# Performance work log

Hardware: AMD Instinct MI355X
Metric: run time of the kernel (lower is better)

## Reference

```python
import jax, jax.numpy as jnp
import numpy as np
from jax.scipy.linalg import expm

N_WIRES = 9
N_LAYERS = 4
EMBED = 512
BATCH = 64
D = 2 ** N_WIRES
P = N_WIRES * N_LAYERS * 2  # gate angles per sample


def _apply_gate(st, g, w):
    # st: (D, 2,...,2) complex64; apply 2x2 gate g on wire w
    st = jnp.moveaxis(st, 1 + w, -1)
    st = st @ g.T  # new[a] = sum_b g[a,b] old[b]
    return jnp.moveaxis(st, -1, 1 + w)


def _apply_cnot(st, c, t):
    st = jnp.moveaxis(st, (1 + c, 1 + t), (-2, -1))
    st = jnp.concatenate([st[..., 0:1, :], st[..., 1:2, ::-1]], axis=-2)
    return jnp.moveaxis(st, (-2, -1), (1 + c, 1 + t))


def _build_unitary(params):
    # simulate circuit on all D basis states at once (identity input)
    st = jnp.eye(D, dtype=jnp.complex64).reshape((D,) + (2,) * N_WIRES)
    idx = 0
    for _ in range(N_LAYERS):
        for w in range(N_WIRES):
            thy = params[idx]
            thz = params[idx + 1]
            idx += 2
            c = jnp.cos(thy * 0.5).astype(jnp.complex64)
            s = jnp.sin(thy * 0.5).astype(jnp.complex64)
            ry = jnp.stack([jnp.stack([c, -s]), jnp.stack([s, c])])
            ep = jnp.exp(0.5j * thz.astype(jnp.complex64))  # exp(i*thz/2)
            zero = jnp.zeros((), jnp.complex64)
            rz = jnp.stack([jnp.stack([jnp.conj(ep), zero]), jnp.stack([zero, ep])])
            st = _apply_gate(st, rz @ ry, w)  # Ry then Rz, fused
        for w in range(N_WIRES - 1):
            st = _apply_cnot(st, w, w + 1)
        st = _apply_cnot(st, N_WIRES - 1, 0)  # ring entangler (n_wires>1)
    # row index = input basis state i -> column i of U; take real part
    return jnp.real(st.reshape(D, D)).T


def _forward(t, w1, b1, w2, b2):
    h = jax.nn.silu(t[:, None] @ w1 + b1)          # (B, EMBED)
    params = h @ w2 + b2                            # (B, P)
    p_sg = jax.lax.stop_gradient(params)            # torch uses .detach() for the circuit
    U_stack = jax.vmap(_build_unitary)(p_sg)        # (B, D, D)
    B = t.shape[0]
    A = jnp.zeros((B, D * D), params.dtype).at[:, :P].set(params).reshape(B, D, D)
    A_skew = (A - jnp.swapaxes(A, -1, -2)) * 0.01
    U_diff = jax.vmap(expm)(A_skew)                 # (B, D, D)
    return jnp.einsum('bij,bjk->bik', U_stack, U_diff)


def setup_inputs() -> dict:
    key = jax.random.key(0)
    k_t, k1, kb1, k2, kb2 = jax.random.split(key, 5)
    t = jax.random.normal(k_t, (BATCH,), jnp.float32)
    w1 = jax.random.normal(k1, (1, EMBED), jnp.float32)
    b1 = jax.random.normal(kb1, (EMBED,), jnp.float32) * 0.1
    w2 = jax.random.normal(k2, (EMBED, P), jnp.float32) / np.sqrt(EMBED)
    b2 = jax.random.normal(kb2, (P,), jnp.float32) * 0.1
    return {"t": t, "w1": w1, "b1": b1, "w2": w2, "b2": b2}


def reference(t, w1, b1, w2, b2):
    return _forward(t, w1, b1, w2, b2)
```

## Files before the change

### kernel.cpp

```cpp
#include <hip/hip_runtime.h>
#include <math.h>


#define PSTRIDE 2560
#define GD_OFF  0
#define SC_OFF  144
#define L_OFF(l) (160 + (l)*256)
#define V_OFF   1184
#define W_OFF   1280
#define C0_OFF  1792

__device__ __forceinline__ float2 cmul(float2 a, float2 b){
  return make_float2(fmaf(a.x, b.x, -a.y*b.y), fmaf(a.x, b.y, a.y*b.x));
}

__device__ __forceinline__ float2 pk_fma_s_lo(float2 s2, float2 b, float2 c){
  float2 d;
  asm("v_pk_fma_f32 %0, %1, %2, %3 op_sel:[0,0,0] op_sel_hi:[0,1,1]"
      : "=v"(d) : "s"(s2), "v"(b), "v"(c));
  return d;
}
__device__ __forceinline__ float2 pk_mul_s_hi(float2 s2, float2 b){
  float2 d;
  asm("v_pk_mul_f32 %0, %1, %2 op_sel:[1,0] op_sel_hi:[1,1]"
      : "=v"(d) : "s"(s2), "v"(b));
  return d;
}
__device__ __forceinline__ float2 pk_mul_s_lo(float2 s2, float2 b){
  float2 d;
  asm("v_pk_mul_f32 %0, %1, %2 op_sel:[0,0] op_sel_hi:[0,1]"
      : "=v"(d) : "s"(s2), "v"(b));
  return d;
}
__device__ __forceinline__ float2 pk_fma_vs_lo(float2 a, float2 b, float2 c){
  float2 d;
  asm("v_pk_fma_f32 %0, %1, %2, %3 op_sel:[0,0,0] op_sel_hi:[0,1,1]"
      : "=v"(d) : "v"(a), "s"(b), "v"(c));
  return d;
}
__device__ __forceinline__ float2 pk_mul_vs_hi(float2 a, float2 b){
  float2 d;
  asm("v_pk_mul_f32 %0, %1, %2 op_sel:[1,0] op_sel_hi:[1,1]"
      : "=v"(d) : "v"(a), "s"(b));
  return d;
}
__device__ __forceinline__ float2 pk_fma_vv_lo(float2 a, float2 b, float2 c){
  float2 d;
  asm("v_pk_fma_f32 %0, %1, %2, %3 op_sel:[0,0,0] op_sel_hi:[0,1,1]"
      : "=v"(d) : "v"(a), "v"(b), "v"(c));
  return d;
}
__device__ __forceinline__ float2 pk_mul_vv_hi(float2 a, float2 b){
  float2 d;
  asm("v_pk_mul_f32 %0, %1, %2 op_sel:[1,0] op_sel_hi:[1,1]"
      : "=v"(d) : "v"(a), "v"(b));
  return d;
}
__device__ __forceinline__ float2 pk_swapneg(float2 c, float2 n){
  float2 d;
  asm("v_pk_mul_f32 %0, %1, %2 op_sel:[1,0] op_sel_hi:[0,1]"
      : "=v"(d) : "v"(c), "v"(n));
  return d;
}

template<int OFS>
__device__ __forceinline__ float2 swz2(float2 v){
  const int x = __builtin_amdgcn_ds_swizzle(__float_as_int(v.x), OFS);
  const int y = __builtin_amdgcn_ds_swizzle(__float_as_int(v.y), OFS);
  return make_float2(__int_as_float(x), __int_as_float(y));
}
template<int CTRL>
__device__ __forceinline__ float2 dpp2(float2 v){
  const int x = __builtin_amdgcn_mov_dpp(__float_as_int(v.x), CTRL, 0xF, 0xF, true);
  const int y = __builtin_amdgcn_mov_dpp(__float_as_int(v.y), CTRL, 0xF, 0xF, true);
  return make_float2(__int_as_float(x), __int_as_float(y));
}

__device__ __forceinline__ int Fperm(int x){
  int S = x ^ (x >> 1); S ^= S >> 2; S ^= S >> 4; S ^= S >> 8;
  return (S & 0xFF) | ((((x >> 8) ^ S) & 1) << 8);
}
__device__ __forceinline__ int physmap(int x){ return x ^ ((x >> 4) & 15); }

template<int STRIDE, bool UNIF>
__device__ __forceinline__ void apply_rot(float2 amp[8], const float* rp){
  const float2 R0 = ((const float2*)rp)[0];
  const float2 R1 = ((const float2*)rp)[1];
  #pragma unroll
  for (int b = 0; b < 8; ++b){
    if (b & STRIDE) continue;
    const float2 u = amp[b], v = amp[b + STRIDE];
    if constexpr (UNIF){
      amp[b]          = pk_fma_s_lo(R0, u, pk_mul_s_hi(R0, v));
      amp[b + STRIDE] = pk_fma_s_lo(R1, u, pk_mul_s_hi(R1, v));
    } else {
      amp[b]          = pk_fma_vv_lo(R0, u, pk_mul_vv_hi(R0, v));
      amp[b + STRIDE] = pk_fma_vv_lo(R1, u, pk_mul_vv_hi(R1, v));
    }
  }
}

__device__ __forceinline__ void run_layer2(float2* __restrict__ S,
    const float* __restrict__ lb, const int lane,
    const int base1, const int base2, const int base3, const int baseF,
    const float2 NEG1P1){
  float2 amp[8];
  #pragma unroll
  for (int j = 0; j < 8; ++j) amp[j] = S[base1 ^ j];
  apply_rot<4,false>(amp, lb + 6*4);
  apply_rot<2,false>(amp, lb + 7*4);
  apply_rot<1,false>(amp, lb + 8*4);
  #pragma unroll
  for (int j = 0; j < 8; ++j) S[base1 ^ j] = amp[j];
  #pragma unroll
  for (int j = 0; j < 8; ++j) amp[j] = S[base2 ^ ((j << 3) ^ (j >> 1))];
  apply_rot<4,false>(amp, lb + 3*4);
  apply_rot<2,false>(amp, lb + 4*4);
  apply_rot<1,false>(amp, lb + 5*4);
  #pragma unroll
  for (int j = 0; j < 8; ++j) S[base2 ^ ((j << 3) ^ (j >> 1))] = amp[j];
  #pragma unroll
  for (int j = 0; j < 8; ++j) amp[j] = S[base3 ^ ((j << 6) ^ ((4*j) & 15))];
  apply_rot<4,false>(amp, lb + 0*4);
  apply_rot<2,false>(amp, lb + 1*4);
  apply_rot<1,false>(amp, lb + 2*4);
  {
    const float2 A  = *(const float2*)(lb + 128 + lane*2);
    const float2 A2 = pk_swapneg(A, NEG1P1);
    #pragma unroll
    for (int j = 0; j < 8; ++j)
      amp[j] = pk_fma_vv_lo(amp[j], A, pk_mul_vv_hi(amp[j], A2));
    #pragma unroll
    for (int j = 0; j < 8; ++j){
      const float2 P = *(const float2*)(lb + 64 + j*4);
      const float2 Q = *(const float2*)(lb + 64 + j*4 + 2);
      amp[j] = pk_fma_vv_lo(amp[j], P, pk_mul_vv_hi(amp[j], Q));
    }
  }
  #pragma unroll
  for (int j = 0; j < 8; ++j) S[baseF ^ physmap(Fperm(j << 6))] = amp[j];
}

#define XROT(GET, RP, BIT) {                                        \
    const float2 R0 = ((const float2*)(RP))[0];    \
    const float2 R1 = ((const float2*)(RP))[1];    \
    const float  Bs = (BIT) ? R1.x : R0.y;                          \
    const float2 Bv = make_float2(Bs, Bs);                          \
    _Pragma("unroll")                                               \
    for (int j = 0; j < 8; ++j){                                    \
      const float2 p = GET(amp[j]);                                 \
      amp[j] = pk_fma_vv_lo(Bv, p, pk_mul_s_lo(R0, amp[j]));        \
    }                                                               \
  }

__device__ __forceinline__ void run_layer_h(float2* __restrict__ S,
    const float* __restrict__ lb, const int lane,
    const int base1, const int base3, const int baseF,
    const float2 NEG1P1){
  float2 amp[8];
  #pragma unroll
  for (int j = 0; j < 8; ++j) amp[j] = S[base1 ^ j];
  apply_rot<4,true>(amp, lb + 6*4);
  apply_rot<2,true>(amp, lb + 7*4);
  apply_rot<1,true>(amp, lb + 8*4);
  XROT(swz2<0x101F>, lb + 3*4, (lane >> 2) & 1);
  XROT(dpp2<0x4E>,   lb + 4*4, (lane >> 1) & 1);
  XROT(dpp2<0xB1>,   lb + 5*4, lane & 1);
  #pragma unroll
  for (int j = 0; j < 8; ++j) S[base1 ^ j] = amp[j];
  #pragma unroll
  for (int j = 0; j < 8; ++j) amp[j] = S[base3 ^ ((j << 6) ^ ((4*j) & 15))];
  apply_rot<4,true>(amp, lb + 0*4);
  apply_rot<2,true>(amp, lb + 1*4);
  apply_rot<1,true>(amp, lb + 2*4);
  {
    const float2 A  = *(const float2*)(lb + 128 + lane*2);
    const float2 A2 = pk_swapneg(A, NEG1P1);
    #pragma unroll
    for (int j = 0; j < 8; ++j)
      amp[j] = pk_fma_vv_lo(amp[j], A, pk_mul_vv_hi(amp[j], A2));
    #pragma unroll
    for (int j = 0; j < 8; ++j){
      const float2 P = *(const float2*)(lb + 64 + j*4);
      const float2 Q = *(const float2*)(lb + 64 + j*4 + 2);
      amp[j] = pk_fma_vs_lo(amp[j], P, pk_mul_vs_hi(amp[j], Q));
    }
  }
  #pragma unroll
  for (int j = 0; j < 8; ++j) S[baseF ^ physmap(Fperm(j << 6))] = amp[j];
}

__global__ __launch_bounds__(576)
void prep_kernel(const float* __restrict__ t,  const float* __restrict__ w1,
                 const float* __restrict__ b1, const float* __restrict__ w2,
                 const float* __restrict__ b2, float* __restrict__ prep){
  __shared__ float sh[512];
  __shared__ float part[8][72];
  __shared__ float spar[72];
  __shared__ float tl[4][256];
  __shared__ float ssc[3];
  __shared__ __align__(16) float2 vst[2][512];
  const int s = blockIdx.x;
  const float ts = t[s];
  for (int k = threadIdx.x; k < 512; k += 576){
    const float z = fmaf(ts, w1[k], b1[k]);
    sh[k] = z / (1.f + expf(-z));
  }
  __syncthreads();
  {
    const int p = threadIdx.x % 72, c = threadIdx.x / 72;
    float acc = 0.f;
    const int k0 = c*64;
    for (int k = k0; k < k0 + 64; ++k) acc = fmaf(sh[k], w2[k*72 + p], acc);
    part[c][p] = acc;
  }
  __syncthreads();
  if (threadIdx.x < 72){
    const int p = threadIdx.x;
    float acc = b2[p];
    #pragma unroll
    for (int c = 0; c < 8; ++c) acc += part[c][p];
    spar[p] = acc;
  }
  __syncthreads();
  float* pb = prep + (size_t)s*PSTRIDE;
  const int tid = threadIdx.x;
  if (tid < 256){
    const int l = tid >> 6, m = tid & 63;
    float2 acc = make_float2(1.f, 0.f);
    #pragma unroll
    for (int w = 3; w < 9; ++w){
      const float thz = spar[2*(9*l + w) + 1];
      float zi, zr; sincosf(0.5f*thz, &zi, &zr);
      const int bit = (m >> (8 - w)) & 1;
      acc = cmul(acc, make_float2(zr, bit ? zi : -zi));
    }
    pb[L_OFF(l) + 128 + 2*m]     = acc.x;
    pb[L_OFF(l) + 128 + 2*m + 1] = acc.y;
    tl[l][128 + 2*m]     = acc.x;
    tl[l][128 + 2*m + 1] = acc.y;
  } else if (tid < 288){
    const int q = tid - 256, l = q >> 3, j = q & 7;
    float2 acc = make_float2(1.f, 0.f);
    #pragma unroll
    for (int w = 0; w < 3; ++w){
      const float thz = spar[2*(9*l + w) + 1];
      float zi, zr; sincosf(0.5f*thz, &zi, &zr);
      const int bit = (j >> (2 - w)) & 1;
      acc = cmul(acc, make_float2(zr, bit ? zi : -zi));
    }
    float* o = pb + L_OFF(l) + 64 + j*4;
    o[0] = acc.x; o[1] = acc.y; o[2] = -acc.y; o[3] = acc.x;
    float* o2 = &tl[l][64 + j*4];
    o2[0] = acc.x; o2[1] = acc.y; o2[2] = -acc.y; o2[3] = acc.x;
  } else if (tid < 324){
    const int q = tid - 288, l = q / 9, w = q - l*9;
    const float thy = spar[2*(9*l + w)];
    float sy, cy; sincosf(0.5f*thy, &sy, &cy);
    float* o = pb + L_OFF(l) + w*4;
    o[0] = cy; o[1] = -sy; o[2] = sy; o[3] = cy;
    float* o2 = &tl[l][w*4];
    o2[0] = cy; o2[1] = -sy; o2[2] = sy; o2[3] = cy;
  } else if (tid < 333){
    const int w = tid - 324;
    const float thy = spar[2*w], thz = spar[2*w + 1];
    float sy, cy, zi, zr;
    sincosf(0.5f*thy, &sy, &cy);
    sincosf(0.5f*thz, &zi, &zr);
    const float gr[4] = { zr*cy, -zr*sy, zr*sy, zr*cy };
    const float gi[4] = { -zi*cy, zi*sy, zi*sy, zi*cy };
    float* o = pb + GD_OFF + w*16;
    #pragma unroll
    for (int e = 0; e < 4; ++e){
      o[e*4+0] = gr[e]; o[e*4+1] = gi[e]; o[e*4+2] = -gi[e]; o[e*4+3] = gr[e];
    }
  } else if (tid < 405){
    const int j = tid - 333;
    pb[V_OFF + j] = (j == 0) ? 0.f : 0.01f*spar[j];
  } else if (tid == 405){
    float th2 = 0.f;
    for (int j = 1; j < 72; ++j){ const float v = 0.01f*spar[j]; th2 = fmaf(v, v, th2); }
    const float th = sqrtf(th2);
    float alpha, beta;
    if (th > 1e-6f){
      alpha = sinf(th)/th;
      const float s2 = sinf(0.5f*th);
      beta = 2.f*s2*s2/th2;
    } else { alpha = 1.f - th2/6.f; beta = 0.5f; }
    pb[SC_OFF+0] = cosf(th);
    pb[SC_OFF+1] = alpha;
    pb[SC_OFF+2] = beta;
    ssc[0] = cosf(th); ssc[1] = alpha; ssc[2] = beta;
  }
  __syncthreads();
  if (tid < 128){
    const int wv = tid >> 6, lane = tid & 63;
    float2* const S = vst[wv];
    const float2 NEG1P1 = make_float2(-1.f, 1.f);
    const int base1 = (lane << 3) ^ ((lane >> 1) & 15);
    const int hq = lane >> 3, lq = lane & 7;
    const int base2 = (hq << 6) ^ ((hq << 2) & 15) ^ lq;
    const int base3 = lane ^ (lane >> 4);
    const int baseF = physmap(Fperm(lane));
    #pragma unroll
    for (int j = 0; j < 8; ++j){
      const int x = (lane << 3) + j;
      float re;
      if (wv == 0) re = (x == 0) ? 1.f : 0.f;
      else         re = (x >= 1 && x < 72) ? 0.01f*spar[x] : 0.f;
      S[base1 ^ j] = make_float2(re, 0.f);
    }
    #pragma unroll
    for (int L = 0; L < 4; ++L)
      run_layer2(S, &tl[L][0], lane, base1, base2, base3, baseF, NEG1P1);
  }
  __syncthreads();
  if (tid < 512){
    const int a  = tid;
    const int pa = a ^ ((a >> 4) & 15);
    const float u0 = vst[0][pa].x;
    const float uv = vst[1][pa].x;
    pb[W_OFF  + a] = fmaf(ssc[1], u0, -ssc[2]*uv);
    pb[C0_OFF + a] = fmaf(ssc[0], u0, -ssc[1]*uv);
  }
}

__global__ __launch_bounds__(512, 6)
void sim_kernel(const float* __restrict__ prep, float* __restrict__ out){
  __shared__ __align__(16) float2 st[8][512];
  const int s    = blockIdx.x & 63;
  const int cb   = blockIdx.x >> 6;
  const int wid  = threadIdx.x >> 6;
  const int lane = threadIdx.x & 63;
  const int col  = cb*8 + wid;
  const float* gp = prep + (size_t)s*PSTRIDE;
  float2* const S = st[wid];
  const float2 NEG1P1 = make_float2(-1.f, 1.f);

  float2 amp[8];
  {
    float2 base = make_float2(1.f, 0.f);
    #pragma unroll
    for (int w = 0; w < 6; ++w){
      const int xb = (lane >> (5 - w)) & 1;
      const int ib = (col  >> (8 - w)) & 1;
      const float4 gd = *(const float4*)(gp + GD_OFF + w*16 + (xb*2 + ib)*4);
      const float2 d1 = make_float2(gd.x, gd.y);
      const float2 d2 = make_float2(gd.z, gd.w);
      base = pk_fma_vv_lo(base, d1, pk_mul_vv_hi(base, d2));
    }
    const int i6 = (col >> 2) & 1, i7 = (col >> 1) & 1, i8 = col & 1;
    float2 g6[2]; float4 g7d[2], g8d[2];
    #pragma unroll
    for (int r = 0; r < 2; ++r){
      g6[r]  = *(const float2*)(gp + GD_OFF + 6*16 + (r*2 + i6)*4);
      g7d[r] = *(const float4*)(gp + GD_OFF + 7*16 + (r*2 + i7)*4);
      g8d[r] = *(const float4*)(gp + GD_OFF + 8*16 + (r*2 + i8)*4);
    }
    float2 g67[4];
    #pragma unroll
    for (int a = 0; a < 2; ++a){
      #pragma unroll
      for (int b = 0; b < 2; ++b){
        const float2 d1 = make_float2(g7d[b].x, g7d[b].y);
        const float2 d2 = make_float2(g7d[b].z, g7d[b].w);
        g67[a*2+b] = pk_fma_vv_lo(g6[a], d1, pk_mul_vv_hi(g6[a], d2));
      }
    }
    const float2 bd2 = pk_swapneg(base, NEG1P1);
    #pragma unroll
    for (int j = 0; j < 8; ++j){
      const float4 g8 = g8d[j & 1];
      const float2 e1 = make_float2(g8.x, g8.y);
      const float2 e2 = make_float2(g8.z, g8.w);
      const float2 T  = pk_fma_vv_lo(g67[j >> 1], e1, pk_mul_vv_hi(g67[j >> 1], e2));
      amp[j] = pk_fma_vv_lo(T, base, pk_mul_vv_hi(T, bd2));
    }
    const int bFI = physmap(Fperm(lane << 3));
    #pragma unroll
    for (int j = 0; j < 8; ++j) S[bFI ^ physmap(Fperm(j))] = amp[j];
  }

  const int base1 = (lane << 3) ^ ((lane >> 1) & 15);
  const int base3 = lane ^ (lane >> 4);
  const int baseF = physmap(Fperm(lane));

  run_layer_h(S, gp + L_OFF(1), lane, base1, base3, baseF, NEG1P1);
  run_layer_h(S, gp + L_OFF(2), lane, base1, base3, baseF, NEG1P1);
  run_layer_h(S, gp + L_OFF(3), lane, base1, base3, baseF, NEG1P1);

  __syncthreads();
  const float* wt  = gp + W_OFF;
  const float* c0t = gp + C0_OFF;
  const float* vt  = gp + V_OFF;
  #pragma unroll
  for (int rep = 0; rep < 2; ++rep){
    const int a  = (threadIdx.x >> 1) + rep*256;
    const int q  = threadIdx.x & 1;
    const int pa = a ^ ((a >> 4) & 15);
    float4 vv;
    vv.x = st[q*4 + 0][pa].x;
    vv.y = st[q*4 + 1][pa].x;
    vv.z = st[q*4 + 2][pa].x;
    vv.w = st[q*4 + 3][pa].x;
    if (cb < 9){
      const float  wa = wt[a];
      const float4 vj = *(const float4*)(vt + cb*8 + q*4);
      vv.x = fmaf(wa, vj.x, vv.x);
      vv.y = fmaf(wa, vj.y, vv.y);
      vv.z = fmaf(wa, vj.z, vv.z);
      vv.w = fmaf(wa, vj.w, vv.w);
      if ((cb | q) == 0) vv.x = c0t[a];
    }
    *(float4*)&out[(size_t)s*262144 + (size_t)a*512 + cb*8 + q*4] = vv;
  }
}

extern "C" void kernel_launch(void* const* d_in, const int* in_sizes, int n_in,
                              void* d_out, int out_size, void* d_ws, size_t ws_size,
                              hipStream_t stream){
  const float* t  = (const float*)d_in[0];
  const float* w1 = (const float*)d_in[1];
  const float* b1 = (const float*)d_in[2];
  const float* w2 = (const float*)d_in[3];
  const float* b2 = (const float*)d_in[4];
  float* out  = (float*)d_out;
  float* prep = (float*)d_ws;
  prep_kernel<<<64,   576, 0, stream>>>(t, w1, b1, w2, b2, prep);
  sim_kernel <<<4096, 512, 0, stream>>>(prep, out);
}
```

Baseline: 143.2 us.

## Replace mid-layer LDS transpose with cross-lane rotations for high wires

New measurement: 146.9 us. 2.6% more time.

```diff
diff --git a/kernel.cpp b/kernel.cpp
--- a/kernel.cpp
+++ b/kernel.cpp
@@ -73,6 +73,11 @@
 __device__ __forceinline__ float2 dpp2(float2 v){
   const int x = __builtin_amdgcn_mov_dpp(__float_as_int(v.x), CTRL, 0xF, 0xF, true);
   const int y = __builtin_amdgcn_mov_dpp(__float_as_int(v.y), CTRL, 0xF, 0xF, true);
+  return make_float2(__int_as_float(x), __int_as_float(y));
+}
+__device__ __forceinline__ float2 bperm2(int addr, float2 v){
+  const int x = __builtin_amdgcn_ds_bpermute(addr, __float_as_int(v.x));
+  const int y = __builtin_amdgcn_ds_bpermute(addr, __float_as_int(v.y));
   return make_float2(__int_as_float(x), __int_as_float(y));
 }
 
@@ -141,21 +146,21 @@
   for (int j = 0; j < 8; ++j) S[baseF ^ physmap(Fperm(j << 6))] = amp[j];
 }
 
-#define XROT(GET, RP, BIT) {                                        \
+#define XROT(GETEXPR, RP, BIT) {                                    \
     const float2 R0 = ((const float2*)(RP))[0];    \
     const float2 R1 = ((const float2*)(RP))[1];    \
     const float  Bs = (BIT) ? R1.x : R0.y;                          \
     const float2 Bv = make_float2(Bs, Bs);                          \
     _Pragma("unroll")                                               \
     for (int j = 0; j < 8; ++j){                                    \
-      const float2 p = GET(amp[j]);                                 \
+      const float2 p = GETEXPR;                                     \
       amp[j] = pk_fma_vv_lo(Bv, p, pk_mul_s_lo(R0, amp[j]));        \
     }                                                               \
   }
 
-__device__ __forceinline__ void run_layer_h(float2* __restrict__ S,
+__device__ __forceinline__ void run_layer_r(float2* __restrict__ S,
     const float* __restrict__ lb, const int lane,
-    const int base1, const int base3, const int baseF,
+    const int base1, const int bFI, const int bpaddr,
     const float2 NEG1P1){
   float2 amp[8];
   #pragma unroll
@@ -163,16 +168,12 @@
   apply_rot<4,true>(amp, lb + 6*4);
   apply_rot<2,true>(amp, lb + 7*4);
   apply_rot<1,true>(amp, lb + 8*4);
-  XROT(swz2<0x101F>, lb + 3*4, (lane >> 2) & 1);
-  XROT(dpp2<0x4E>,   lb + 4*4, (lane >> 1) & 1);
-  XROT(dpp2<0xB1>,   lb + 5*4, lane & 1);
-  #pragma unroll
-  for (int j = 0; j < 8; ++j) S[base1 ^ j] = amp[j];
-  #pragma unroll
-  for (int j = 0; j < 8; ++j) amp[j] = S[base3 ^ ((j << 6) ^ ((4*j) & 15))];
-  apply_rot<4,true>(amp, lb + 0*4);
-  apply_rot<2,true>(amp, lb + 1*4);
-  apply_rot<1,true>(amp, lb + 2*4);
+  XROT(swz2<0x101F>(amp[j]), lb + 3*4, (lane >> 2) & 1);
+  XROT(dpp2<0x4E>(amp[j]),   lb + 4*4, (lane >> 1) & 1);
+  XROT(dpp2<0xB1>(amp[j]),   lb + 5*4, lane & 1);
+  XROT(bperm2(bpaddr, amp[j]), lb + 0*4, (lane >> 5) & 1);
+  XROT(swz2<0x401F>(amp[j]),   lb + 1*4, (lane >> 4) & 1);
+  XROT(swz2<0x201F>(amp[j]),   lb + 2*4, (lane >> 3) & 1);
   {
     const float2 A  = *(const float2*)(lb + 128 + lane*2);
     const float2 A2 = pk_swapneg(A, NEG1P1);
@@ -187,7 +188,7 @@
     }
   }
   #pragma unroll
-  for (int j = 0; j < 8; ++j) S[baseF ^ physmap(Fperm(j << 6))] = amp[j];
+  for (int j = 0; j < 8; ++j) S[bFI ^ physmap(Fperm(j))] = amp[j];
 }
 
 __global__ __launch_bounds__(576)
@@ -235,10 +236,18 @@
       const int bit = (m >> (8 - w)) & 1;
       acc = cmul(acc, make_float2(zr, bit ? zi : -zi));
     }
-    pb[L_OFF(l) + 128 + 2*m]     = acc.x;
-    pb[L_OFF(l) + 128 + 2*m + 1] = acc.y;
     tl[l][128 + 2*m]     = acc.x;
     tl[l][128 + 2*m + 1] = acc.y;
+    float2 dl = make_float2(1.f, 0.f);
+    #pragma unroll
+    for (int w = 0; w < 6; ++w){
+      const float thz = spar[2*(9*l + w) + 1];
+      float zi, zr; sincosf(0.5f*thz, &zi, &zr);
+      const int bit = (m >> (5 - w)) & 1;
+      dl = cmul(dl, make_float2(zr, bit ? zi : -zi));
+    }
+    pb[L_OFF(l) + 128 + 2*m]     = dl.x;
+    pb[L_OFF(l) + 128 + 2*m + 1] = dl.y;
   } else if (tid < 288){
     const int q = tid - 256, l = q >> 3, j = q & 7;
     float2 acc = make_float2(1.f, 0.f);
@@ -249,10 +258,18 @@
       const int bit = (j >> (2 - w)) & 1;
       acc = cmul(acc, make_float2(zr, bit ? zi : -zi));
     }
-    float* o = pb + L_OFF(l) + 64 + j*4;
-    o[0] = acc.x; o[1] = acc.y; o[2] = -acc.y; o[3] = acc.x;
     float* o2 = &tl[l][64 + j*4];
     o2[0] = acc.x; o2[1] = acc.y; o2[2] = -acc.y; o2[3] = acc.x;
+    float2 dj = make_float2(1.f, 0.f);
+    #pragma unroll
+    for (int w = 6; w < 9; ++w){
+      const float thz = spar[2*(9*l + w) + 1];
+      float zi, zr; sincosf(0.5f*thz, &zi, &zr);
+      const int bit = (j >> (8 - w)) & 1;
+      dj = cmul(dj, make_float2(zr, bit ? zi : -zi));
+    }
+    float* o = pb + L_OFF(l) + 64 + j*4;
+    o[0] = dj.x; o[1] = dj.y; o[2] = -dj.y; o[3] = dj.x;
   } else if (tid < 324){
     const int q = tid - 288, l = q / 9, w = q - l*9;
     const float thy = spar[2*(9*l + w)];
@@ -338,6 +355,7 @@
   const float2 NEG1P1 = make_float2(-1.f, 1.f);
 
   float2 amp[8];
+  const int bFI = physmap(Fperm(lane << 3));
   {
     float2 base = make_float2(1.f, 0.f);
     #pragma unroll
@@ -376,18 +394,16 @@
       const float2 T  = pk_fma_vv_lo(g67[j >> 1], e1, pk_mul_vv_hi(g67[j >> 1], e2));
       amp[j] = pk_fma_vv_lo(T, base, pk_mul_vv_hi(T, bd2));
     }
-    const int bFI = physmap(Fperm(lane << 3));
     #pragma unroll
     for (int j = 0; j < 8; ++j) S[bFI ^ physmap(Fperm(j))] = amp[j];
   }
 
-  const int base1 = (lane << 3) ^ ((lane >> 1) & 15);
-  const int base3 = lane ^ (lane >> 4);
-  const int baseF = physmap(Fperm(lane));
-
-  run_layer_h(S, gp + L_OFF(1), lane, base1, base3, baseF, NEG1P1);
-  run_layer_h(S, gp + L_OFF(2), lane, base1, base3, baseF, NEG1P1);
-  run_layer_h(S, gp + L_OFF(3), lane, base1, base3, baseF, NEG1P1);
+  const int base1  = (lane << 3) ^ ((lane >> 1) & 15);
+  const int bpaddr = (lane ^ 32) << 2;
+
+  run_layer_r(S, gp + L_OFF(1), lane, base1, bFI, bpaddr, NEG1P1);
+  run_layer_r(S, gp + L_OFF(2), lane, base1, bFI, bpaddr, NEG1P1);
+  run_layer_r(S, gp + L_OFF(3), lane, base1, bFI, bpaddr, NEG1P1);
 
   __syncthreads();
   const float* wt  = gp + W_OFF;
```
